# Optimization experiments

Measured on AMD Instinct MI355X. Metric: run time of the kernel, lower is better.

## Reference

```python
import jax, jax.numpy as jnp
import numpy as np

NEG_SLOPE = 0.2       # PyG GATConv default leaky_relu negative_slope
NUM_GRAPHS = 128
VOCAB, HID, HEADS, NCLS = 5000, 64, 4, 20
N_NODES, N_EDGES = 50000, 1600000


def gat_conv(x, src, dst, W, a_src, a_dst, bias, concat):
    """PyG-style GATConv (eval mode, self-loops already in src/dst).
    W: [in, H*C]; a_src/a_dst: [H, C]; bias: [H*C] if concat else [C]."""
    N = x.shape[0]
    H, C = a_src.shape
    h = (x @ W).reshape(N, H, C)                      # [N,H,C]
    al_src = jnp.sum(h * a_src, axis=-1)              # [N,H]
    al_dst = jnp.sum(h * a_dst, axis=-1)              # [N,H]
    e = al_src[src] + al_dst[dst]                     # [E,H]
    e = jnp.where(e > 0, e, NEG_SLOPE * e)            # leaky_relu
    # segment softmax over incoming edges of each dst node
    emax = jax.lax.stop_gradient(jax.ops.segment_max(e, dst, num_segments=N))
    emax = jnp.where(jnp.isfinite(emax), emax, 0.0)
    ex = jnp.exp(e - emax[dst])
    denom = jax.ops.segment_sum(ex, dst, num_segments=N)
    alpha = ex / (denom[dst] + 1e-16)                 # [E,H]
    out = jax.ops.segment_sum(h[src] * alpha[..., None], dst, num_segments=N)  # [N,H,C]
    out = out.reshape(N, H * C) if concat else out.mean(axis=1)
    return out + bias


def setup_inputs() -> dict:
    key = jax.random.key(0)
    ks = jax.random.split(key, 12)
    C1 = HID // HEADS

    def xavier(k, shape):
        fan_in, fan_out = shape[0], shape[-1]
        lim = np.sqrt(6.0 / (fan_in + fan_out))
        return jax.random.uniform(k, shape, jnp.float32, -lim, lim)

    return {
        "x": jax.random.normal(ks[0], (N_NODES, VOCAB), jnp.float32),
        "edge_index": jax.random.randint(ks[1], (2, N_EDGES), 0, N_NODES, jnp.int32),
        "batch": jnp.sort(jax.random.randint(ks[2], (N_NODES,), 0, NUM_GRAPHS, jnp.int32)),
        "W1": xavier(ks[3], (VOCAB, HID)),
        "a_src1": xavier(ks[4], (HEADS, C1)),
        "a_dst1": xavier(ks[5], (HEADS, C1)),
        "b1": jnp.zeros((HID,), jnp.float32),
        "W2": xavier(ks[6], (HID, HID)),
        "a_src2": xavier(ks[7], (1, HID)),
        "a_dst2": xavier(ks[8], (1, HID)),
        "b2": jnp.zeros((HID,), jnp.float32),
        "Wc": xavier(ks[9], (HID, NCLS)),
        "bc": jnp.zeros((NCLS,), jnp.float32),
    }


def reference(x, edge_index, batch, W1, a_src1, a_dst1, b1,
              W2, a_src2, a_dst2, b2, Wc, bc):
    N = x.shape[0]
    loop = jnp.arange(N, dtype=edge_index.dtype)
    src = jnp.concatenate([edge_index[0], loop])      # add self-loops (PyG default)
    dst = jnp.concatenate([edge_index[1], loop])

    h = jax.nn.elu(gat_conv(x, src, dst, W1, a_src1, a_dst1, b1, concat=True))
    h = jax.nn.elu(gat_conv(h, src, dst, W2, a_src2, a_dst2, b2, concat=False))

    # global_mean_pool over batch ids
    sums = jax.ops.segment_sum(h, batch, num_segments=NUM_GRAPHS)           # [G,HID]
    cnts = jax.ops.segment_sum(jnp.ones((N, 1), h.dtype), batch, num_segments=NUM_GRAPHS)
    pooled = sums / jnp.maximum(cnts, 1.0)

    logits = pooled @ Wc + bc
    return jax.nn.log_softmax(logits, axis=1)
```

## Files before the change

kernel.cpp:

```cpp
#include <hip/hip_runtime.h>

#define N_NODES 50000
#define VOCAB   5000
#define HID     64
#define HEADS   4
#define NCLS    20
#define NGRAPH  128
#define N_EDGES 1600000
#define ETOT    (N_EDGES + N_NODES)

typedef __attribute__((ext_vector_type(8))) short short8;
typedef __attribute__((ext_vector_type(4))) float f32x4;

__device__ inline ushort f2bf(float x) {
  union { float f; unsigned u; } c; c.f = x;
  unsigned r = (c.u + 0x7fffu + ((c.u >> 16) & 1u)) >> 16;
  return (ushort)r;
}

__global__ void cvt_bf16_kernel(const float* __restrict__ in, ushort* __restrict__ out, int n) {
  int i = blockIdx.x * blockDim.x + threadIdx.x;
  if (i < n) out[i] = f2bf(in[i]);
}

template<int KT>
__global__ __launch_bounds__(256) void gemm_kernel(const float* __restrict__ A,
    const ushort* __restrict__ B, float* __restrict__ D, int M) {
  __shared__ ushort As[64][40];
  __shared__ ushort Bs[64][40];
  int t = threadIdx.x;
  int wave = t >> 6, lane = t & 63;
  int lr = lane & 15, quad = lane >> 4;
  int rowBase = blockIdx.x * 64;
  f32x4 acc[4] = {{0,0,0,0},{0,0,0,0},{0,0,0,0},{0,0,0,0}};
  const int KSTEPS = (KT + 31) / 32;
  for (int ks = 0; ks < KSTEPS; ++ks) {
    int k0 = ks * 32;
    __syncthreads();
    #pragma unroll
    for (int i = 0; i < 2; ++i) {
      int q = t + i * 256;
      int row = q >> 3, c4 = (q & 7) << 2;
      float4 v = make_float4(0.f, 0.f, 0.f, 0.f);
      int gr = rowBase + row;
      if (gr < M && (k0 + c4) < KT)
        v = *(const float4*)(A + (size_t)gr * KT + k0 + c4);
      ushort4 u;
      u.x = f2bf(v.x); u.y = f2bf(v.y); u.z = f2bf(v.z); u.w = f2bf(v.w);
      *(ushort4*)&As[row][c4] = u;
    }
    {
      int e0 = t << 3;
      int k = e0 >> 6, c = e0 & 63;
      union { uint4 v; ushort u[8]; } w;
      w.v = make_uint4(0, 0, 0, 0);
      if (k0 + k < KT)
        w.v = *(const uint4*)(B + (size_t)(k0 + k) * 64 + c);
      #pragma unroll
      for (int j = 0; j < 8; ++j) Bs[c + j][k] = w.u[j];
    }
    __syncthreads();
    short8 af = *(short8*)&As[wave * 16 + lr][quad * 8];
    #pragma unroll
    for (int ct = 0; ct < 4; ++ct) {
      short8 bfr = *(short8*)&Bs[ct * 16 + lr][quad * 8];
      acc[ct] = __builtin_amdgcn_mfma_f32_16x16x32_bf16(af, bfr, acc[ct], 0, 0, 0);
    }
  }
  #pragma unroll
  for (int ct = 0; ct < 4; ++ct) {
    #pragma unroll
    for (int r = 0; r < 4; ++r) {
      int grow = rowBase + wave * 16 + quad * 4 + r;
      if (grow < M) D[(size_t)grow * 64 + ct * 16 + lr] = acc[ct][r];
    }
  }
}

__global__ void al_h4_kernel(const float* __restrict__ h, const float* __restrict__ a_src,
                             const float* __restrict__ a_dst, float* __restrict__ alS,
                             float* __restrict__ alD, int n) {
  int wid = (blockIdx.x * blockDim.x + threadIdx.x) >> 6;
  int lane = threadIdx.x & 63;
  if (wid >= n) return;
  float hv = h[(size_t)wid * 64 + lane];
  float s = hv * a_src[lane];
  float d = hv * a_dst[lane];
  #pragma unroll
  for (int off = 1; off < 16; off <<= 1) {
    s += __shfl_down(s, off, 16);
    d += __shfl_down(d, off, 16);
  }
  if ((lane & 15) == 0) {
    alS[wid * 4 + (lane >> 4)] = s;
    alD[wid * 4 + (lane >> 4)] = d;
  }
}

__global__ void al_h1_kernel(const float* __restrict__ h, const float* __restrict__ a_src,
                             const float* __restrict__ a_dst, float* __restrict__ alS,
                             float* __restrict__ alD, int n) {
  int wid = (blockIdx.x * blockDim.x + threadIdx.x) >> 6;
  int lane = threadIdx.x & 63;
  if (wid >= n) return;
  float hv = h[(size_t)wid * 64 + lane];
  float s = hv * a_src[lane];
  float d = hv * a_dst[lane];
  #pragma unroll
  for (int off = 1; off < 64; off <<= 1) {
    s += __shfl_down(s, off, 64);
    d += __shfl_down(d, off, 64);
  }
  if (lane == 0) { alS[wid] = s; alD[wid] = d; }
}

__global__ void hist_kernel(const int* __restrict__ dstA, int* __restrict__ deg, int E, int Etot) {
  int i = blockIdx.x * blockDim.x + threadIdx.x;
  if (i >= Etot) return;
  int d = (i < E) ? dstA[i] : (i - E);
  atomicAdd(&deg[d], 1);
}

#define SCAN_T 1024
__global__ __launch_bounds__(SCAN_T) void scan_kernel(const int* __restrict__ deg,
                                                      int* __restrict__ indptr, int n) {
  __shared__ int buf[SCAN_T];
  __shared__ int s_run;
  int t = threadIdx.x;
  if (t == 0) s_run = 0;
  __syncthreads();
  for (int base = 0; base < n; base += SCAN_T) {
    int i = base + t;
    int v = (i < n) ? deg[i] : 0;
    buf[t] = v;
    __syncthreads();
    for (int off = 1; off < SCAN_T; off <<= 1) {
      int x = (t >= off) ? buf[t - off] : 0;
      __syncthreads();
      buf[t] += x;
      __syncthreads();
    }
    int incl = buf[t];
    int total = buf[SCAN_T - 1];
    if (i < n) indptr[i] = s_run + incl - v;
    __syncthreads();
    if (t == 0) s_run += total;
    __syncthreads();
  }
  if (t == 0) indptr[n] = s_run;
}

__global__ void scatter_kernel(const int* __restrict__ srcA, const int* __restrict__ dstA,
                               const int* __restrict__ indptr, int* __restrict__ fill,
                               int* __restrict__ srcs, int E, int Etot) {
  int i = blockIdx.x * blockDim.x + threadIdx.x;
  if (i >= Etot) return;
  int d, s;
  if (i < E) { d = dstA[i]; s = srcA[i]; } else { d = i - E; s = d; }
  int pos = indptr[d] + atomicAdd(&fill[d], 1);
  srcs[pos] = s;
}

template<int H>
__global__ void agg_kernel(const float* __restrict__ h, const float* __restrict__ alS,
                           const float* __restrict__ alD, const int* __restrict__ indptr,
                           const int* __restrict__ srcs, const float* __restrict__ bias,
                           float* __restrict__ out, int n) {
  int wid = (blockIdx.x * blockDim.x + threadIdx.x) >> 6;
  int lane = threadIdx.x & 63;
  if (wid >= n) return;
  constexpr int C = 64 / H;
  int head = lane / C;
  float ald = alD[wid * H + head];
  int j0 = indptr[wid], j1 = indptr[wid + 1];
  float m = -3.0e38f, ssum = 0.f, acc = 0.f;
  for (int j = j0; j < j1; ++j) {
    int s = srcs[j];
    float e = alS[s * H + head] + ald;
    e = e > 0.f ? e : 0.2f * e;
    float hv = h[(size_t)s * 64 + lane];
    float mn = fmaxf(m, e);
    float sc = __expf(m - mn);
    float p  = __expf(e - mn);
    ssum = ssum * sc + p;
    acc  = acc * sc + p * hv;
    m = mn;
  }
  float o = acc / (ssum + 1e-16f) + bias[lane];
  o = o > 0.f ? o : __expf(o) - 1.f;
  out[(size_t)wid * 64 + lane] = o;
}

__global__ void cnt_kernel(const int* __restrict__ batch, int* __restrict__ cnts, int n) {
  int i = blockIdx.x * blockDim.x + threadIdx.x;
  if (i < n) atomicAdd(&cnts[batch[i]], 1);
}

__global__ void pool_kernel(const float* __restrict__ h, const int* __restrict__ batch,
                            float* __restrict__ pooled, int n) {
  int wid = (blockIdx.x * blockDim.x + threadIdx.x) >> 6;
  int lane = threadIdx.x & 63;
  int n0 = wid * 64;
  if (n0 >= n) return;
  int n1 = min(n0 + 64, n);
  int g_cur = batch[n0];
  float acc = 0.f;
  for (int i = n0; i < n1; ++i) {
    int g = batch[i];
    if (g != g_cur) {
      atomicAdd(&pooled[g_cur * 64 + lane], acc);
      acc = 0.f; g_cur = g;
    }
    acc += h[(size_t)i * 64 + lane];
  }
  atomicAdd(&pooled[g_cur * 64 + lane], acc);
}

__global__ __launch_bounds__(128) void cls_kernel(const float* __restrict__ pooled,
    const int* __restrict__ cnts, const float* __restrict__ Wc,
    const float* __restrict__ bc, float* __restrict__ out) {
  int g = threadIdx.x;
  if (g >= NGRAPH) return;
  float inv = 1.f / fmaxf((float)cnts[g], 1.f);
  float p[64];
  #pragma unroll
  for (int k = 0; k < 64; ++k) p[k] = pooled[g * 64 + k] * inv;
  float lg[NCLS];
  float mx = -3.0e38f;
  #pragma unroll
  for (int c = 0; c < NCLS; ++c) {
    float v = bc[c];
    for (int k = 0; k < 64; ++k) v += p[k] * Wc[k * NCLS + c];
    lg[c] = v;
    mx = fmaxf(mx, v);
  }
  float se = 0.f;
  #pragma unroll
  for (int c = 0; c < NCLS; ++c) se += expf(lg[c] - mx);
  float ls = logf(se);
  #pragma unroll
  for (int c = 0; c < NCLS; ++c) out[g * NCLS + c] = lg[c] - mx - ls;
}

extern "C" void kernel_launch(void* const* d_in, const int* in_sizes, int n_in,
                              void* d_out, int out_size, void* d_ws, size_t ws_size,
                              hipStream_t stream) {
  const float* x      = (const float*)d_in[0];
  const int*   ei     = (const int*)d_in[1];
  const int*   batch  = (const int*)d_in[2];
  const float* W1     = (const float*)d_in[3];
  const float* a_src1 = (const float*)d_in[4];
  const float* a_dst1 = (const float*)d_in[5];
  const float* b1     = (const float*)d_in[6];
  const float* W2     = (const float*)d_in[7];
  const float* a_src2 = (const float*)d_in[8];
  const float* a_dst2 = (const float*)d_in[9];
  const float* b2     = (const float*)d_in[10];
  const float* Wc     = (const float*)d_in[11];
  const float* bc     = (const float*)d_in[12];
  float* out = (float*)d_out;

  const int* srcA = ei;
  const int* dstA = ei + N_EDGES;

  char* ws = (char*)d_ws;
  size_t off = 0;
  auto alloc = [&](size_t bytes) -> void* {
    void* p = ws + off;
    off = (off + bytes + 255) & ~(size_t)255;
    return p;
  };
  float* bufA   = (float*)alloc((size_t)N_NODES * 64 * 4);
  float* bufB   = (float*)alloc((size_t)N_NODES * 64 * 4);
  float* alS1   = (float*)alloc((size_t)N_NODES * 4 * 4);
  float* alD1   = (float*)alloc((size_t)N_NODES * 4 * 4);
  float* alS2   = (float*)alloc((size_t)N_NODES * 4);
  float* alD2   = (float*)alloc((size_t)N_NODES * 4);
  ushort* w1bf  = (ushort*)alloc((size_t)VOCAB * 64 * 2);
  ushort* w2bf  = (ushort*)alloc((size_t)64 * 64 * 2);
  int* deg      = (int*)alloc((size_t)N_NODES * 4);
  int* fill     = (int*)alloc((size_t)N_NODES * 4);
  int* indptr   = (int*)alloc((size_t)(N_NODES + 1) * 4);
  int* srcs     = (int*)alloc((size_t)ETOT * 4);
  float* pooled = (float*)alloc((size_t)NGRAPH * 64 * 4);
  int* cnts     = (int*)alloc((size_t)NGRAPH * 4);

  hipMemsetAsync(deg, 0, (size_t)N_NODES * 4, stream);
  hipMemsetAsync(fill, 0, (size_t)N_NODES * 4, stream);
  hipMemsetAsync(pooled, 0, (size_t)NGRAPH * 64 * 4, stream);
  hipMemsetAsync(cnts, 0, (size_t)NGRAPH * 4, stream);

  cvt_bf16_kernel<<<(VOCAB * 64 + 255) / 256, 256, 0, stream>>>(W1, w1bf, VOCAB * 64);
  cvt_bf16_kernel<<<(64 * 64 + 255) / 256, 256, 0, stream>>>(W2, w2bf, 64 * 64);

  int egrid = (ETOT + 255) / 256;
  hist_kernel<<<egrid, 256, 0, stream>>>(dstA, deg, N_EDGES, ETOT);
  scan_kernel<<<1, SCAN_T, 0, stream>>>(deg, indptr, N_NODES);
  scatter_kernel<<<egrid, 256, 0, stream>>>(srcA, dstA, indptr, fill, srcs, N_EDGES, ETOT);

  int nwaveBlocks = (N_NODES * 64 + 255) / 256;

  gemm_kernel<VOCAB><<<(N_NODES + 63) / 64, 256, 0, stream>>>(x, w1bf, bufA, N_NODES);
  al_h4_kernel<<<nwaveBlocks, 256, 0, stream>>>(bufA, a_src1, a_dst1, alS1, alD1, N_NODES);
  agg_kernel<4><<<nwaveBlocks, 256, 0, stream>>>(bufA, alS1, alD1, indptr, srcs, b1, bufB, N_NODES);

  gemm_kernel<64><<<(N_NODES + 63) / 64, 256, 0, stream>>>(bufB, w2bf, bufA, N_NODES);
  al_h1_kernel<<<nwaveBlocks, 256, 0, stream>>>(bufA, a_src2, a_dst2, alS2, alD2, N_NODES);
  agg_kernel<1><<<nwaveBlocks, 256, 0, stream>>>(bufA, alS2, alD2, indptr, srcs, b2, bufB, N_NODES);

  cnt_kernel<<<(N_NODES + 255) / 256, 256, 0, stream>>>(batch, cnts, N_NODES);
  pool_kernel<<<((N_NODES + 63) / 64 * 64 + 255) / 256, 256, 0, stream>>>(bufB, batch, pooled, N_NODES);
  cls_kernel<<<1, 128, 0, stream>>>(pooled, cnts, Wc, bc, out);
}
```

Before: 2.181 ms.

## Stream GEMM without LDS, shuffle-based scan, unrolled aggregation and fast pooling

Replaces the LDS-tiled GEMM with a per-wave streaming GEMM. Each wave reads fp32 A rows directly into MFMA fragments and reads a pre-transposed, K-padded bf16 weight, which removes the shared-memory staging and barriers. Also rewrites the scan with wave shuffles, unrolls the GAT aggregation by four with prefetched source indices, and adds a fast path in pooling when a 64-node chunk lies in one graph. Risks include less data reuse of the weight across waves (it relies on the cache) and reads past the end of the CSR source array, which is covered by padding srcs.

```diff
diff --git a/kernel.cpp b/kernel.cpp
--- a/kernel.cpp
+++ b/kernel.cpp
@@ -2,6 +2,7 @@
 
 #define N_NODES 50000
 #define VOCAB   5000
+#define KPAD1   5024
 #define HID     64
 #define HEADS   4
 #define NCLS    20
@@ -18,63 +19,67 @@
   return (ushort)r;
 }
 
-__global__ void cvt_bf16_kernel(const float* __restrict__ in, ushort* __restrict__ out, int n) {
+__global__ void cvtT_kernel(const float* __restrict__ W, ushort* __restrict__ Bt,
+                            int K, int KP) {
   int i = blockIdx.x * blockDim.x + threadIdx.x;
-  if (i < n) out[i] = f2bf(in[i]);
-}
-
-template<int KT>
-__global__ __launch_bounds__(256) void gemm_kernel(const float* __restrict__ A,
-    const ushort* __restrict__ B, float* __restrict__ D, int M) {
-  __shared__ ushort As[64][40];
-  __shared__ ushort Bs[64][40];
-  int t = threadIdx.x;
-  int wave = t >> 6, lane = t & 63;
+  if (i >= 64 * KP) return;
+  int n = i / KP, k = i - n * KP;
+  Bt[i] = (k < K) ? f2bf(W[(size_t)k * 64 + n]) : (ushort)0;
+}
+
+template<int KT, int KP>
+__global__ __launch_bounds__(256) void gemm_stream(const float* __restrict__ A,
+    const ushort* __restrict__ Bt, float* __restrict__ D, int M) {
+  int gt = blockIdx.x * 256 + threadIdx.x;
+  int gw = gt >> 6, lane = gt & 63;
   int lr = lane & 15, quad = lane >> 4;
-  int rowBase = blockIdx.x * 64;
+  int m0 = gw * 16;
+  if (m0 >= M) return;
+  const float*  ap = A  + (size_t)(m0 + lr) * KT + quad * 8;
+  const ushort* bp = Bt + (size_t)lr * KP + quad * 8;
   f32x4 acc[4] = {{0,0,0,0},{0,0,0,0},{0,0,0,0},{0,0,0,0}};
-  const int KSTEPS = (KT + 31) / 32;
-  for (int ks = 0; ks < KSTEPS; ++ks) {
-    int k0 = ks * 32;
-    __syncthreads();
+  constexpr int KF = (KT / 32) * 32;
+  #pragma unroll 2
+  for (int k0 = 0; k0 < KF; k0 += 32) {
+    float4 v0 = *(const float4*)(ap + k0);
+    float4 v1 = *(const float4*)(ap + k0 + 4);
+    short8 b0 = *(const short8*)(bp + k0);
+    short8 b1 = *(const short8*)(bp + 16 * KP + k0);
+    short8 b2 = *(const short8*)(bp + 32 * KP + k0);
+    short8 b3 = *(const short8*)(bp + 48 * KP + k0);
+    short8 af;
+    af[0] = (short)f2bf(v0.x); af[1] = (short)f2bf(v0.y);
+    af[2] = (short)f2bf(v0.z); af[3] = (short)f2bf(v0.w);
+    af[4] = (short)f2bf(v1.x); af[5] = (short)f2bf(v1.y);
+    af[6] = (short)f2bf(v1.z); af[7] = (short)f2bf(v1.w);
+    acc[0] = __builtin_amdgcn_mfma_f32_16x16x32_bf16(af, b0, acc[0], 0, 0, 0);
+    acc[1] = __builtin_amdgcn_mfma_f32_16x16x32_bf16(af, b1, acc[1], 0, 0, 0);
+    acc[2] = __builtin_amdgcn_mfma_f32_16x16x32_bf16(af, b2, acc[2], 0, 0, 0);
+    acc[3] = __builtin_amdgcn_mfma_f32_16x16x32_bf16(af, b3, acc[3], 0, 0, 0);
+  }
+  if (KT % 32) {
+    int k0 = KF;
+    float4 v0 = make_float4(0,0,0,0), v1 = make_float4(0,0,0,0);
+    if (quad == 0) { v0 = *(const float4*)(ap + k0); v1 = *(const float4*)(ap + k0 + 4); }
+    short8 b0 = *(const short8*)(bp + k0);
+    short8 b1 = *(const short8*)(bp + 16 * KP + k0);
+    short8 b2 = *(const short8*)(bp + 32 * KP + k0);
+    short8 b3 = *(const short8*)(bp + 48 * KP + k0);
+    short8 af;
+    af[0] = (short)f2bf(v0.x); af[1] = (short)f2bf(v0.y);
+    af[2] = (short)f2bf(v0.z); af[3] = (short)f2bf(v0.w);
+    af[4] = (short)f2bf(v1.x); af[5] = (short)f2bf(v1.y);
+    af[6] = (short)f2bf(v1.z); af[7] = (short)f2bf(v1.w);
+    acc[0] = __builtin_amdgcn_mfma_f32_16x16x32_bf16(af, b0, acc[0], 0, 0, 0);
+    acc[1] = __builtin_amdgcn_mfma_f32_16x16x32_bf16(af, b1, acc[1], 0, 0, 0);
+    acc[2] = __builtin_amdgcn_mfma_f32_16x16x32_bf16(af, b2, acc[2], 0, 0, 0);
+    acc[3] = __builtin_amdgcn_mfma_f32_16x16x32_bf16(af, b3, acc[3], 0, 0, 0);
+  }
+  #pragma unroll
+  for (int ct = 0; ct < 4; ++ct)
     #pragma unroll
-    for (int i = 0; i < 2; ++i) {
-      int q = t + i * 256;
-      int row = q >> 3, c4 = (q & 7) << 2;
-      float4 v = make_float4(0.f, 0.f, 0.f, 0.f);
-      int gr = rowBase + row;
-      if (gr < M && (k0 + c4) < KT)
-        v = *(const float4*)(A + (size_t)gr * KT + k0 + c4);
-      ushort4 u;
-      u.x = f2bf(v.x); u.y = f2bf(v.y); u.z = f2bf(v.z); u.w = f2bf(v.w);
-      *(ushort4*)&As[row][c4] = u;
-    }
-    {
-      int e0 = t << 3;
-      int k = e0 >> 6, c = e0 & 63;
-      union { uint4 v; ushort u[8]; } w;
-      w.v = make_uint4(0, 0, 0, 0);
-      if (k0 + k < KT)
-        w.v = *(const uint4*)(B + (size_t)(k0 + k) * 64 + c);
-      #pragma unroll
-      for (int j = 0; j < 8; ++j) Bs[c + j][k] = w.u[j];
-    }
-    __syncthreads();
-    short8 af = *(short8*)&As[wave * 16 + lr][quad * 8];
-    #pragma unroll
-    for (int ct = 0; ct < 4; ++ct) {
-      short8 bfr = *(short8*)&Bs[ct * 16 + lr][quad * 8];
-      acc[ct] = __builtin_amdgcn_mfma_f32_16x16x32_bf16(af, bfr, acc[ct], 0, 0, 0);
-    }
-  }
-  #pragma unroll
-  for (int ct = 0; ct < 4; ++ct) {
-    #pragma unroll
-    for (int r = 0; r < 4; ++r) {
-      int grow = rowBase + wave * 16 + quad * 4 + r;
-      if (grow < M) D[(size_t)grow * 64 + ct * 16 + lr] = acc[ct][r];
-    }
-  }
+    for (int r = 0; r < 4; ++r)
+      D[(size_t)(m0 + quad * 4 + r) * 64 + ct * 16 + lr] = acc[ct][r];
 }
 
 __global__ void al_h4_kernel(const float* __restrict__ h, const float* __restrict__ a_src,
@@ -121,33 +126,41 @@
   atomicAdd(&deg[d], 1);
 }
 
-#define SCAN_T 1024
-__global__ __launch_bounds__(SCAN_T) void scan_kernel(const int* __restrict__ deg,
-                                                      int* __restrict__ indptr, int n) {
-  __shared__ int buf[SCAN_T];
-  __shared__ int s_run;
-  int t = threadIdx.x;
-  if (t == 0) s_run = 0;
+__global__ __launch_bounds__(1024) void scan_kernel(const int* __restrict__ deg,
+                                                    int* __restrict__ indptr, int n) {
+  __shared__ int wsum[16];
+  __shared__ int carry;
+  int t = threadIdx.x, w = t >> 6, lane = t & 63;
+  if (t == 0) carry = 0;
   __syncthreads();
-  for (int base = 0; base < n; base += SCAN_T) {
+  for (int base = 0; base < n; base += 1024) {
     int i = base + t;
     int v = (i < n) ? deg[i] : 0;
-    buf[t] = v;
+    int x = v;
+    #pragma unroll
+    for (int off = 1; off < 64; off <<= 1) {
+      int y = __shfl_up(x, off, 64);
+      if (lane >= off) x += y;
+    }
+    if (lane == 63) wsum[w] = x;
     __syncthreads();
-    for (int off = 1; off < SCAN_T; off <<= 1) {
-      int x = (t >= off) ? buf[t - off] : 0;
-      __syncthreads();
-      buf[t] += x;
-      __syncthreads();
+    if (w == 0 && lane < 16) {
+      int y = wsum[lane];
+      #pragma unroll
+      for (int off = 1; off < 16; off <<= 1) {
+        int z = __shfl_up(y, off, 16);
+        if (lane >= off) y += z;
+      }
+      wsum[lane] = y;
     }
-    int incl = buf[t];
-    int total = buf[SCAN_T - 1];
-    if (i < n) indptr[i] = s_run + incl - v;
     __syncthreads();
-    if (t == 0) s_run += total;
+    int incl = x + (w > 0 ? wsum[w - 1] : 0) + carry;
+    if (i < n) indptr[i] = incl - v;
     __syncthreads();
-  }
-  if (t == 0) indptr[n] = s_run;
+    if (t == 1023) carry = incl;
+    __syncthreads();
+  }
+  if (t == 0) indptr[n] = carry;
 }
 
 __global__ void scatter_kernel(const int* __restrict__ srcA, const int* __restrict__ dstA,
@@ -162,10 +175,10 @@
 }
 
 template<int H>
-__global__ void agg_kernel(const float* __restrict__ h, const float* __restrict__ alS,
-                           const float* __restrict__ alD, const int* __restrict__ indptr,
-                           const int* __restrict__ srcs, const float* __restrict__ bias,
-                           float* __restrict__ out, int n) {
+__global__ __launch_bounds__(256) void agg_kernel(const float* __restrict__ h,
+    const float* __restrict__ alS, const float* __restrict__ alD,
+    const int* __restrict__ indptr, const int* __restrict__ srcs,
+    const float* __restrict__ bias, float* __restrict__ out, int n) {
   int wid = (blockIdx.x * blockDim.x + threadIdx.x) >> 6;
   int lane = threadIdx.x & 63;
   if (wid >= n) return;
@@ -174,16 +187,37 @@
   float ald = alD[wid * H + head];
   int j0 = indptr[wid], j1 = indptr[wid + 1];
   float m = -3.0e38f, ssum = 0.f, acc = 0.f;
-  for (int j = j0; j < j1; ++j) {
-    int s = srcs[j];
-    float e = alS[s * H + head] + ald;
-    e = e > 0.f ? e : 0.2f * e;
-    float hv = h[(size_t)s * 64 + lane];
-    float mn = fmaxf(m, e);
+  int p0 = srcs[j0], p1 = srcs[j0 + 1], p2 = srcs[j0 + 2], p3 = srcs[j0 + 3];
+  for (int j = j0; j < j1; j += 4) {
+    int rem = j1 - j;
+    int s0 = p0;
+    int s1 = (rem > 1) ? p1 : p0;
+    int s2 = (rem > 2) ? p2 : p0;
+    int s3 = (rem > 3) ? p3 : p0;
+    int jn = j + 4;
+    if (jn < j1) { p0 = srcs[jn]; p1 = srcs[jn + 1]; p2 = srcs[jn + 2]; p3 = srcs[jn + 3]; }
+    float e0 = alS[s0 * H + head] + ald;
+    float e1 = alS[s1 * H + head] + ald;
+    float e2 = alS[s2 * H + head] + ald;
+    float e3 = alS[s3 * H + head] + ald;
+    float h0 = h[(size_t)s0 * 64 + lane];
+    float h1 = h[(size_t)s1 * 64 + lane];
+    float h2 = h[(size_t)s2 * 64 + lane];
+    float h3 = h[(size_t)s3 * 64 + lane];
+    e0 = e0 > 0.f ? e0 : 0.2f * e0;
+    e1 = e1 > 0.f ? e1 : 0.2f * e1;
+    e2 = e2 > 0.f ? e2 : 0.2f * e2;
+    e3 = e3 > 0.f ? e3 : 0.2f * e3;
+    e1 = (rem > 1) ? e1 : -3.0e38f;
+    e2 = (rem > 2) ? e2 : -3.0e38f;
+    e3 = (rem > 3) ? e3 : -3.0e38f;
+    float cm = fmaxf(fmaxf(e0, e1), fmaxf(e2, e3));
+    float mn = fmaxf(m, cm);
     float sc = __expf(m - mn);
-    float p  = __expf(e - mn);
-    ssum = ssum * sc + p;
-    acc  = acc * sc + p * hv;
+    float q0 = __expf(e0 - mn), q1 = __expf(e1 - mn);
+    float q2 = __expf(e2 - mn), q3 = __expf(e3 - mn);
+    ssum = ssum * sc + q0 + q1 + q2 + q3;
+    acc  = acc  * sc + q0 * h0 + q1 * h1 + q2 * h2 + q3 * h3;
     m = mn;
   }
   float o = acc / (ssum + 1e-16f) + bias[lane];
@@ -203,17 +237,26 @@
   int n0 = wid * 64;
   if (n0 >= n) return;
   int n1 = min(n0 + 64, n);
-  int g_cur = batch[n0];
-  float acc = 0.f;
-  for (int i = n0; i < n1; ++i) {
-    int g = batch[i];
-    if (g != g_cur) {
-      atomicAdd(&pooled[g_cur * 64 + lane], acc);
-      acc = 0.f; g_cur = g;
+  int g = batch[min(n0 + lane, n - 1)];
+  int gf = __shfl(g, 0), gl = __shfl(g, 63);
+  if (gf == gl && n1 == n0 + 64) {
+    float a = 0.f;
+    #pragma unroll 8
+    for (int i = n0; i < n1; ++i) a += h[(size_t)i * 64 + lane];
+    atomicAdd(&pooled[gf * 64 + lane], a);
+  } else {
+    int g_cur = batch[n0];
+    float a = 0.f;
+    for (int i = n0; i < n1; ++i) {
+      int gg = batch[i];
+      if (gg != g_cur) {
+        atomicAdd(&pooled[g_cur * 64 + lane], a);
+        a = 0.f; g_cur = gg;
+      }
+      a += h[(size_t)i * 64 + lane];
     }
-    acc += h[(size_t)i * 64 + lane];
-  }
-  atomicAdd(&pooled[g_cur * 64 + lane], acc);
+    atomicAdd(&pooled[g_cur * 64 + lane], a);
+  }
 }
 
 __global__ __launch_bounds__(128) void cls_kernel(const float* __restrict__ pooled,
@@ -276,12 +319,12 @@
   float* alD1   = (float*)alloc((size_t)N_NODES * 4 * 4);
   float* alS2   = (float*)alloc((size_t)N_NODES * 4);
   float* alD2   = (float*)alloc((size_t)N_NODES * 4);
-  ushort* w1bf  = (ushort*)alloc((size_t)VOCAB * 64 * 2);
-  ushort* w2bf  = (ushort*)alloc((size_t)64 * 64 * 2);
+  ushort* w1t   = (ushort*)alloc((size_t)64 * KPAD1 * 2);
+  ushort* w2t   = (ushort*)alloc((size_t)64 * 64 * 2);
   int* deg      = (int*)alloc((size_t)N_NODES * 4);
   int* fill     = (int*)alloc((size_t)N_NODES * 4);
   int* indptr   = (int*)alloc((size_t)(N_NODES + 1) * 4);
-  int* srcs     = (int*)alloc((size_t)ETOT * 4);
+  int* srcs     = (int*)alloc((size_t)(ETOT + 16) * 4);
   float* pooled = (float*)alloc((size_t)NGRAPH * 64 * 4);
   int* cnts     = (int*)alloc((size_t)NGRAPH * 4);
 
@@ -290,21 +333,22 @@
   hipMemsetAsync(pooled, 0, (size_t)NGRAPH * 64 * 4, stream);
   hipMemsetAsync(cnts, 0, (size_t)NGRAPH * 4, stream);
 
-  cvt_bf16_kernel<<<(VOCAB * 64 + 255) / 256, 256, 0, stream>>>(W1, w1bf, VOCAB * 64);
-  cvt_bf16_kernel<<<(64 * 64 + 255) / 256, 256, 0, stream>>>(W2, w2bf, 64 * 64);
+  cvtT_kernel<<<(64 * KPAD1 + 255) / 256, 256, 0, stream>>>(W1, w1t, VOCAB, KPAD1);
+  cvtT_kernel<<<(64 * 64 + 255) / 256, 256, 0, stream>>>(W2, w2t, 64, 64);
 
   int egrid = (ETOT + 255) / 256;
   hist_kernel<<<egrid, 256, 0, stream>>>(dstA, deg, N_EDGES, ETOT);
-  scan_kernel<<<1, SCAN_T, 0, stream>>>(deg, indptr, N_NODES);
+  scan_kernel<<<1, 1024, 0, stream>>>(deg, indptr, N_NODES);
   scatter_kernel<<<egrid, 256, 0, stream>>>(srcA, dstA, indptr, fill, srcs, N_EDGES, ETOT);
 
   int nwaveBlocks = (N_NODES * 64 + 255) / 256;
-
-  gemm_kernel<VOCAB><<<(N_NODES + 63) / 64, 256, 0, stream>>>(x, w1bf, bufA, N_NODES);
+  int gemmBlocks = ((N_NODES + 15) / 16 + 3) / 4;
+
+  gemm_stream<VOCAB, KPAD1><<<gemmBlocks, 256, 0, stream>>>(x, w1t, bufA, N_NODES);
   al_h4_kernel<<<nwaveBlocks, 256, 0, stream>>>(bufA, a_src1, a_dst1, alS1, alD1, N_NODES);
   agg_kernel<4><<<nwaveBlocks, 256, 0, stream>>>(bufA, alS1, alD1, indptr, srcs, b1, bufB, N_NODES);
 
-  gemm_kernel<64><<<(N_NODES + 63) / 64, 256, 0, stream>>>(bufB, w2bf, bufA, N_NODES);
+  gemm_stream<64, 64><<<gemmBlocks, 256, 0, stream>>>(bufB, w2t, bufA, N_NODES);
   al_h1_kernel<<<nwaveBlocks, 256, 0, stream>>>(bufA, a_src2, a_dst2, alS2, alD2, N_NODES);
   agg_kernel<1><<<nwaveBlocks, 256, 0, stream>>>(bufA, alS2, alD2, indptr, srcs, b2, bufB, N_NODES);
 
```

Result: faster. 1.995 ms (-8.5%).
